# Kernel tuning notes

Hardware: AMD Instinct MI355X
Metric: run time of the kernel (lower is better)

Reference implementation:

```python
import jax, jax.numpy as jnp
import numpy as np

KH, KW = 3, 3
STRIDE = 1
OUT_C = 512


def im2col(x, kh, kw, stride):
    # x: [N, C, H, W] -> col: [C*kh*kw, N*oh*ow]  (row order: C major, then kh, kw)
    N, C, H, W = x.shape
    oh = (H - kh) // stride + 1
    ow = (W - kw) // stride + 1
    rows = jnp.arange(oh)[:, None] * stride + jnp.arange(kh)[None, :]  # [oh, kh]
    cols = jnp.arange(ow)[:, None] * stride + jnp.arange(kw)[None, :]  # [ow, kw]
    # gather windows: result [N, C, oh, kh, ow, kw]
    A = x[:, :, rows[:, :, None, None], cols[None, None, :, :]]
    # permute to (C, kh, kw, N, oh, ow) then flatten, matching torch permute(1,4,5,0,2,3)
    col = jnp.transpose(A, (1, 3, 5, 0, 2, 4)).reshape(C * kh * kw, N * oh * ow)
    return col, oh, ow


def setup_inputs() -> dict:
    key = jax.random.key(0)
    k1, k2, k3 = jax.random.split(key, 3)
    N, C, H, W = 16, 256, 32, 32
    K_sel = (C * KH * KW) // 2  # 1152 rows kept by the binary mask
    x = jax.random.normal(k1, (N, C, H, W), dtype=jnp.float32)
    weight = jax.random.normal(k2, (K_sel, OUT_C), dtype=jnp.float32) * 0.02
    idx = jnp.sort(jax.random.randint(k3, (K_sel,), 0, C * KH * KW, dtype=jnp.int32))
    return {"x": x, "weight": weight, "idx": idx}


def reference(x, weight, idx):
    N = x.shape[0]
    col, oh, ow = im2col(x, KH, KW, STRIDE)          # [C*kh*kw, N*oh*ow]
    x_tile = col[idx, :].T                            # gather masked rows -> [N*oh*ow, K_sel]
    conv_out = x_tile @ weight                        # [N*oh*ow, out_c]
    conv_out = conv_out.reshape(N, oh * ow, OUT_C)
    conv_out = jnp.transpose(conv_out, (0, 2, 1)).reshape(N, OUT_C, oh, ow)
    return conv_out
```

## Files before the change

### kernel.cpp

```cpp
#include <hip/hip_runtime.h>
#include <stdint.h>

#define N_IMG   16
#define C_IN    256
#define H_IN    32
#define W_IN    32
#define OH      30
#define OW      30
#define K_SEL   1152
#define OUTC    512
#define RY_TOT  (N_IMG * OH)
#define M_HAT   (RY_TOT * 32)
#define X_ELEMS (N_IMG * C_IN * H_IN * W_IN)
#define OUT_SP  (OH * OW)
#define CHW     (C_IN * H_IN * W_IN)

#define TO      128
#define TM      64
#define NMT     (M_HAT / TM)
#define NOT     (OUTC / TO)
#define BSTR    40
#define KITER   (K_SEL / 32)

typedef float f32x4  __attribute__((ext_vector_type(4)));
typedef short bf16x8 __attribute__((ext_vector_type(8)));

__device__ __forceinline__ unsigned short f2bf(float f) {
    unsigned int u = __float_as_uint(f);
    u += 0x7FFFu + ((u >> 16) & 1u);
    return (unsigned short)(u >> 16);
}

__device__ __forceinline__ void gl_lds16(const void* g, void* lds) {
    __builtin_amdgcn_global_load_lds(
        (const __attribute__((address_space(1))) unsigned int*)g,
        (__attribute__((address_space(3))) unsigned int*)lds,
        16, 0, 0);
}

__global__ void prep_kernel(const int* __restrict__ idx, const float* __restrict__ w,
                            int* __restrict__ koff, unsigned short* __restrict__ wT) {
    __shared__ float tile[32][33];
    const int bx = blockIdx.x, by = blockIdx.y, t = threadIdx.x;

    if (by == 0) {
        int k = bx * 256 + t;
        if (k < K_SEL) {
            int v = idx[k];
            int c = v / 9, rem = v - c * 9;
            int i = rem / 3, j = rem - i * 3;
            koff[k] = c * (H_IN * W_IN) + i * W_IN + j;
        }
    }
    const int s0 = bx * 32, o0 = by * 32;
    const int oc = t & 31, sg = t >> 5;
#pragma unroll
    for (int i = 0; i < 4; ++i) {
        int sl = sg * 4 + i;
        tile[sl][oc] = w[(s0 + sl) * OUTC + o0 + oc];
    }
    __syncthreads();
    const int ol = t >> 3, sq = t & 7;
    unsigned int u0 = (unsigned int)f2bf(tile[sq * 4 + 0][ol]) |
                      ((unsigned int)f2bf(tile[sq * 4 + 1][ol]) << 16);
    unsigned int u1 = (unsigned int)f2bf(tile[sq * 4 + 2][ol]) |
                      ((unsigned int)f2bf(tile[sq * 4 + 3][ol]) << 16);
    uint2 pk; pk.x = u0; pk.y = u1;
    *reinterpret_cast<uint2*>(&wT[(size_t)(o0 + ol) * K_SEL + s0 + sq * 4]) = pk;
}

__global__ __launch_bounds__(256, 4)
void gemm_kernel(const unsigned short* __restrict__ wT, const float* __restrict__ x,
                 const int* __restrict__ koff, float* __restrict__ out) {
    __shared__ __align__(16) unsigned short As[TO * 32];
    __shared__ __align__(16) unsigned short Bs[TM * BSTR];
    __shared__ int koS[K_SEL];

    const int t    = threadIdx.x;
    const int wave = t >> 6;
    const int lane = t & 63;
    const int quad = lane >> 4;
    const int lo   = lane & 15;

    const int bid = blockIdx.x;
    const int mt  = bid % NMT;
    const int ot  = bid / NMT;
    const int oBase = ot * TO;
    const int mBase = mt * TM;

    for (int i = t; i < K_SEL; i += 256) koS[i] = koff[i];

    int base[2];
#pragma unroll
    for (int ry = 0; ry < 2; ++ry) {
        int ryg = mt * 2 + ry;
        int n = ryg / 30, y = ryg - n * 30;
        base[ry] = n * CHW + y * W_IN;
    }

    const int xw  = t & 31;
    const int kq4 = t >> 5;
    const int ks  = kq4 * 4;

    const int lrow = lane >> 2, lks = (lane & 3) * 8;
    const unsigned short* wrow0 = wT + (size_t)(oBase + wave * 32 + lrow) * K_SEL + lks;
    const unsigned short* wrow1 = wrow0 + (size_t)16 * K_SEL;
    unsigned short* lA0 = &As[(wave * 32) * 32];
    unsigned short* lA1 = lA0 + 16 * 32;

    __syncthreads();

    f32x4 acc[2][4] = {};
    int   kk[2][4];
    float v[2][2][4];

#pragma unroll
    for (int j = 0; j < 4; ++j) kk[0][j] = koS[ks + j];
#pragma unroll
    for (int ry = 0; ry < 2; ++ry)
#pragma unroll
        for (int j = 0; j < 4; ++j) {
            int g = base[ry] + kk[0][j] + xw;
            g = min(g, X_ELEMS - 1);
            v[0][ry][j] = x[g];
        }

#pragma unroll 2
    for (int kt = 0; kt < KITER; ++kt) {
        const int p = kt & 1, q = p ^ 1;
        const int k0 = kt * 32;
        gl_lds16(wrow0 + k0, lA0);
        gl_lds16(wrow1 + k0, lA1);
#pragma unroll
        for (int ry = 0; ry < 2; ++ry) {
            unsigned int u0 = (unsigned int)f2bf(v[p][ry][0]) |
                              ((unsigned int)f2bf(v[p][ry][1]) << 16);
            unsigned int u1 = (unsigned int)f2bf(v[p][ry][2]) |
                              ((unsigned int)f2bf(v[p][ry][3]) << 16);
            uint2 pk; pk.x = u0; pk.y = u1;
            *reinterpret_cast<uint2*>(&Bs[(ry * 32 + xw) * BSTR + ks]) = pk;
        }
        if (kt + 1 < KITER) {
            const int k1 = k0 + 32;
#pragma unroll
            for (int j = 0; j < 4; ++j) kk[q][j] = koS[k1 + ks + j];
#pragma unroll
            for (int ry = 0; ry < 2; ++ry)
#pragma unroll
                for (int j = 0; j < 4; ++j) {
                    int g = base[ry] + kk[q][j] + xw;
                    g = min(g, X_ELEMS - 1);
                    v[q][ry][j] = x[g];
                }
        }
        __syncthreads();

        bf16x8 a[2], b[4];
#pragma unroll
        for (int ms = 0; ms < 2; ++ms)
            a[ms] = *(const bf16x8*)&As[(wave * 32 + ms * 16 + lo) * 32 + quad * 8];
#pragma unroll
        for (int ns = 0; ns < 4; ++ns)
            b[ns] = *(const bf16x8*)&Bs[(ns * 16 + lo) * BSTR + quad * 8];
#pragma unroll
        for (int ms = 0; ms < 2; ++ms)
#pragma unroll
            for (int ns = 0; ns < 4; ++ns)
                acc[ms][ns] = __builtin_amdgcn_mfma_f32_16x16x32_bf16(
                    a[ms], b[ns], acc[ms][ns], 0, 0, 0);
        __syncthreads();
    }

#pragma unroll
    for (int ns = 0; ns < 4; ++ns) {
        const int mh  = mBase + ns * 16 + lo;
        const int xwe = mh & 31;
        const int ryg = mh >> 5;
        const int n = ryg / 30, y = ryg - n * 30;
        if (xwe < OW) {
            const size_t ob = (size_t)n * (OUTC * OUT_SP) + (size_t)y * OW + xwe;
#pragma unroll
            for (int ms = 0; ms < 2; ++ms) {
                const int o0 = oBase + wave * 32 + ms * 16 + quad * 4;
#pragma unroll
                for (int r = 0; r < 4; ++r)
                    out[ob + (size_t)(o0 + r) * OUT_SP] = acc[ms][ns][r];
            }
        }
    }
}

extern "C" void kernel_launch(void* const* d_in, const int* in_sizes, int n_in,
                              void* d_out, int out_size, void* d_ws, size_t ws_size,
                              hipStream_t stream) {
    const float* x   = (const float*)d_in[0];
    const float* w   = (const float*)d_in[1];
    const int*   idx = (const int*)d_in[2];
    float*       out = (float*)d_out;

    char* ws = (char*)d_ws;
    int*            koff = (int*)ws;
    unsigned short* wT   = (unsigned short*)(ws + 4608);

    prep_kernel<<<dim3(K_SEL / 32, OUTC / 32), dim3(256), 0, stream>>>(idx, w, koff, wT);
    gemm_kernel<<<dim3(NMT * NOT), dim3(256), 0, stream>>>(wT, x, koff, out);
}
```

Baseline: 113.5 us.

## Double output-channel tile to 256 and reorder gather prefetch before LDS store

Widens the per-block output-channel tile from 128 to 256, so each wave computes a 64x64 accumulator block and the gathered im2col activations are reused across twice as many output channels. This halves redundant x gathers and bf16 conversions across blocks. It also loads the koff offsets as int4, issues the next-iteration x gather before writing the current B tile, and uses the HIP float2-to-bf16 conversion intrinsic. In exchange, register pressure rises, the occupancy hint drops from 4 to 2, and the grid shrinks to 480 blocks, which may leave some CUs with uneven work.

```diff
diff --git a/kernel.cpp b/kernel.cpp
--- a/kernel.cpp
+++ b/kernel.cpp
@@ -1,4 +1,5 @@
 #include <hip/hip_runtime.h>
+#include <hip/hip_bf16.h>
 #include <stdint.h>
 
 #define N_IMG   16
@@ -15,7 +16,7 @@
 #define OUT_SP  (OH * OW)
 #define CHW     (C_IN * H_IN * W_IN)
 
-#define TO      128
+#define TO      256
 #define TM      64
 #define NMT     (M_HAT / TM)
 #define NOT     (OUTC / TO)
@@ -69,12 +70,12 @@
     *reinterpret_cast<uint2*>(&wT[(size_t)(o0 + ol) * K_SEL + s0 + sq * 4]) = pk;
 }
 
-__global__ __launch_bounds__(256, 4)
+__global__ __launch_bounds__(256, 2)
 void gemm_kernel(const unsigned short* __restrict__ wT, const float* __restrict__ x,
                  const int* __restrict__ koff, float* __restrict__ out) {
     __shared__ __align__(16) unsigned short As[TO * 32];
     __shared__ __align__(16) unsigned short Bs[TM * BSTR];
-    __shared__ int koS[K_SEL];
+    __shared__ __align__(16) int koS[K_SEL];
 
     const int t    = threadIdx.x;
     const int wave = t >> 6;
@@ -90,80 +91,74 @@
 
     for (int i = t; i < K_SEL; i += 256) koS[i] = koff[i];
 
-    int base[2];
+    const int xw  = t & 31;
+    const int ks  = (t >> 5) * 4;
+
+    int bxy[2];
 #pragma unroll
     for (int ry = 0; ry < 2; ++ry) {
         int ryg = mt * 2 + ry;
         int n = ryg / 30, y = ryg - n * 30;
-        base[ry] = n * CHW + y * W_IN;
-    }
-
-    const int xw  = t & 31;
-    const int kq4 = t >> 5;
-    const int ks  = kq4 * 4;
-
-    const int lrow = lane >> 2, lks = (lane & 3) * 8;
-    const unsigned short* wrow0 = wT + (size_t)(oBase + wave * 32 + lrow) * K_SEL + lks;
-    const unsigned short* wrow1 = wrow0 + (size_t)16 * K_SEL;
-    unsigned short* lA0 = &As[(wave * 32) * 32];
-    unsigned short* lA1 = lA0 + 16 * 32;
+        bxy[ry] = n * CHW + y * W_IN + xw;
+    }
+
+    const unsigned short* wrowB = wT + (size_t)(oBase + wave * 16 + (lane >> 2)) * K_SEL
+                                     + (lane & 3) * 8;
+    unsigned short* lA = &As[(wave * 16) * 32];
 
     __syncthreads();
 
-    f32x4 acc[2][4] = {};
-    int   kk[2][4];
+    f32x4 acc[4][4] = {};
+    int4  kk[2];
     float v[2][2][4];
 
-#pragma unroll
-    for (int j = 0; j < 4; ++j) kk[0][j] = koS[ks + j];
-#pragma unroll
-    for (int ry = 0; ry < 2; ++ry)
-#pragma unroll
-        for (int j = 0; j < 4; ++j) {
-            int g = base[ry] + kk[0][j] + xw;
-            g = min(g, X_ELEMS - 1);
-            v[0][ry][j] = x[g];
-        }
-
-#pragma unroll 2
+    kk[0] = *reinterpret_cast<const int4*>(&koS[ks]);
+#pragma unroll
+    for (int ry = 0; ry < 2; ++ry) {
+        v[0][ry][0] = x[min(bxy[ry] + kk[0].x, X_ELEMS - 1)];
+        v[0][ry][1] = x[min(bxy[ry] + kk[0].y, X_ELEMS - 1)];
+        v[0][ry][2] = x[min(bxy[ry] + kk[0].z, X_ELEMS - 1)];
+        v[0][ry][3] = x[min(bxy[ry] + kk[0].w, X_ELEMS - 1)];
+    }
+
     for (int kt = 0; kt < KITER; ++kt) {
         const int p = kt & 1, q = p ^ 1;
         const int k0 = kt * 32;
-        gl_lds16(wrow0 + k0, lA0);
-        gl_lds16(wrow1 + k0, lA1);
+#pragma unroll
+        for (int i = 0; i < 4; ++i)
+            gl_lds16(wrowB + (size_t)i * 64 * K_SEL + k0, lA + i * 64 * 32);
+
+        if (kt + 1 < KITER) {
+            kk[q] = *reinterpret_cast<const int4*>(&koS[k0 + 32 + ks]);
+#pragma unroll
+            for (int ry = 0; ry < 2; ++ry) {
+                v[q][ry][0] = x[min(bxy[ry] + kk[q].x, X_ELEMS - 1)];
+                v[q][ry][1] = x[min(bxy[ry] + kk[q].y, X_ELEMS - 1)];
+                v[q][ry][2] = x[min(bxy[ry] + kk[q].z, X_ELEMS - 1)];
+                v[q][ry][3] = x[min(bxy[ry] + kk[q].w, X_ELEMS - 1)];
+            }
+        }
 #pragma unroll
         for (int ry = 0; ry < 2; ++ry) {
-            unsigned int u0 = (unsigned int)f2bf(v[p][ry][0]) |
-                              ((unsigned int)f2bf(v[p][ry][1]) << 16);
-            unsigned int u1 = (unsigned int)f2bf(v[p][ry][2]) |
-                              ((unsigned int)f2bf(v[p][ry][3]) << 16);
+            __hip_bfloat162 h0 = __float22bfloat162_rn({v[p][ry][0], v[p][ry][1]});
+            __hip_bfloat162 h1 = __float22bfloat162_rn({v[p][ry][2], v[p][ry][3]});
+            unsigned int u0, u1;
+            __builtin_memcpy(&u0, &h0, 4);
+            __builtin_memcpy(&u1, &h1, 4);
             uint2 pk; pk.x = u0; pk.y = u1;
             *reinterpret_cast<uint2*>(&Bs[(ry * 32 + xw) * BSTR + ks]) = pk;
         }
-        if (kt + 1 < KITER) {
-            const int k1 = k0 + 32;
-#pragma unroll
-            for (int j = 0; j < 4; ++j) kk[q][j] = koS[k1 + ks + j];
-#pragma unroll
-            for (int ry = 0; ry < 2; ++ry)
-#pragma unroll
-                for (int j = 0; j < 4; ++j) {
-                    int g = base[ry] + kk[q][j] + xw;
-                    g = min(g, X_ELEMS - 1);
-                    v[q][ry][j] = x[g];
-                }
-        }
         __syncthreads();
 
-        bf16x8 a[2], b[4];
-#pragma unroll
-        for (int ms = 0; ms < 2; ++ms)
-            a[ms] = *(const bf16x8*)&As[(wave * 32 + ms * 16 + lo) * 32 + quad * 8];
+        bf16x8 a[4], b[4];
+#pragma unroll
+        for (int ms = 0; ms < 4; ++ms)
+            a[ms] = *(const bf16x8*)&As[(wave * 64 + ms * 16 + lo) * 32 + quad * 8];
 #pragma unroll
         for (int ns = 0; ns < 4; ++ns)
             b[ns] = *(const bf16x8*)&Bs[(ns * 16 + lo) * BSTR + quad * 8];
 #pragma unroll
-        for (int ms = 0; ms < 2; ++ms)
+        for (int ms = 0; ms < 4; ++ms)
 #pragma unroll
             for (int ns = 0; ns < 4; ++ns)
                 acc[ms][ns] = __builtin_amdgcn_mfma_f32_16x16x32_bf16(
@@ -180,8 +175,8 @@
         if (xwe < OW) {
             const size_t ob = (size_t)n * (OUTC * OUT_SP) + (size_t)y * OW + xwe;
 #pragma unroll
-            for (int ms = 0; ms < 2; ++ms) {
-                const int o0 = oBase + wave * 32 + ms * 16 + quad * 4;
+            for (int ms = 0; ms < 4; ++ms) {
+                const int o0 = oBase + wave * 64 + ms * 16 + quad * 4;
 #pragma unroll
                 for (int r = 0; r < 4; ++r)
                     out[ob + (size_t)(o0 + r) * OUT_SP] = acc[ms][ns][r];
```

Result: slower. 144.3 us (+27.2%).

## Double-buffer LDS tiles and prefetch gathered inputs two stages ahead

Applied to the files above, without the earlier changes.

The single LDS A/B tiles become two ping-pong buffers. Each k-step now stages the next tile (async weight loads plus the bf16-packed gathered inputs) while MFMAs run on the current buffer, and the global gather for the tile after that is issued early. This removes one of the two barriers per iteration and hides more global and LDS latency behind compute. In exchange it doubles the A/B shared memory, which can lower occupancy, and it changes how each wave splits the weight-row loads.

```diff
diff --git a/kernel.cpp b/kernel.cpp
--- a/kernel.cpp
+++ b/kernel.cpp
@@ -1,4 +1,5 @@
 #include <hip/hip_runtime.h>
+#include <hip/hip_bf16.h>
 #include <stdint.h>
 
 #define N_IMG   16
@@ -72,9 +73,9 @@
 __global__ __launch_bounds__(256, 4)
 void gemm_kernel(const unsigned short* __restrict__ wT, const float* __restrict__ x,
                  const int* __restrict__ koff, float* __restrict__ out) {
-    __shared__ __align__(16) unsigned short As[TO * 32];
-    __shared__ __align__(16) unsigned short Bs[TM * BSTR];
-    __shared__ int koS[K_SEL];
+    __shared__ __align__(16) unsigned short As[2][TO * 32];
+    __shared__ __align__(16) unsigned short Bs[2][TM * BSTR];
+    __shared__ __align__(16) int koS[K_SEL];
 
     const int t    = threadIdx.x;
     const int wave = t >> 6;
@@ -90,85 +91,100 @@
 
     for (int i = t; i < K_SEL; i += 256) koS[i] = koff[i];
 
-    int base[2];
+    const int xw = t & 31;
+    const int ks = (t >> 5) * 4;
+
+    int bxy[2];
 #pragma unroll
     for (int ry = 0; ry < 2; ++ry) {
         int ryg = mt * 2 + ry;
         int n = ryg / 30, y = ryg - n * 30;
-        base[ry] = n * CHW + y * W_IN;
-    }
-
-    const int xw  = t & 31;
-    const int kq4 = t >> 5;
-    const int ks  = kq4 * 4;
+        bxy[ry] = n * CHW + y * W_IN + xw;
+    }
 
     const int lrow = lane >> 2, lks = (lane & 3) * 8;
-    const unsigned short* wrow0 = wT + (size_t)(oBase + wave * 32 + lrow) * K_SEL + lks;
-    const unsigned short* wrow1 = wrow0 + (size_t)16 * K_SEL;
-    unsigned short* lA0 = &As[(wave * 32) * 32];
-    unsigned short* lA1 = lA0 + 16 * 32;
+    const unsigned short* wrow0 = wT + (size_t)(oBase + wave * 16 + lrow) * K_SEL + lks;
+    const unsigned short* wrow1 = wrow0 + (size_t)64 * K_SEL;
+    const int lA0 = (wave * 16) * 32;
+    const int lA1 = (64 + wave * 16) * 32;
 
     __syncthreads();
 
     f32x4 acc[2][4] = {};
-    int   kk[2][4];
     float v[2][2][4];
-
-#pragma unroll
-    for (int j = 0; j < 4; ++j) kk[0][j] = koS[ks + j];
-#pragma unroll
-    for (int ry = 0; ry < 2; ++ry)
-#pragma unroll
-        for (int j = 0; j < 4; ++j) {
-            int g = base[ry] + kk[0][j] + xw;
-            g = min(g, X_ELEMS - 1);
-            v[0][ry][j] = x[g];
-        }
-
-#pragma unroll 2
+    int4  kk;
+
+    kk = *reinterpret_cast<const int4*>(&koS[ks]);
+#pragma unroll
+    for (int ry = 0; ry < 2; ++ry) {
+        v[0][ry][0] = x[min(bxy[ry] + kk.x, X_ELEMS - 1)];
+        v[0][ry][1] = x[min(bxy[ry] + kk.y, X_ELEMS - 1)];
+        v[0][ry][2] = x[min(bxy[ry] + kk.z, X_ELEMS - 1)];
+        v[0][ry][3] = x[min(bxy[ry] + kk.w, X_ELEMS - 1)];
+    }
+    gl_lds16(wrow0, &As[0][lA0]);
+    gl_lds16(wrow1, &As[0][lA1]);
+#pragma unroll
+    for (int ry = 0; ry < 2; ++ry) {
+        __hip_bfloat162 h0 = __float22bfloat162_rn({v[0][ry][0], v[0][ry][1]});
+        __hip_bfloat162 h1 = __float22bfloat162_rn({v[0][ry][2], v[0][ry][3]});
+        uint2 pk;
+        __builtin_memcpy(&pk.x, &h0, 4);
+        __builtin_memcpy(&pk.y, &h1, 4);
+        *reinterpret_cast<uint2*>(&Bs[0][(ry * 32 + xw) * BSTR + ks]) = pk;
+    }
+    kk = *reinterpret_cast<const int4*>(&koS[32 + ks]);
+#pragma unroll
+    for (int ry = 0; ry < 2; ++ry) {
+        v[1][ry][0] = x[min(bxy[ry] + kk.x, X_ELEMS - 1)];
+        v[1][ry][1] = x[min(bxy[ry] + kk.y, X_ELEMS - 1)];
+        v[1][ry][2] = x[min(bxy[ry] + kk.z, X_ELEMS - 1)];
+        v[1][ry][3] = x[min(bxy[ry] + kk.w, X_ELEMS - 1)];
+    }
+    __syncthreads();
+
     for (int kt = 0; kt < KITER; ++kt) {
         const int p = kt & 1, q = p ^ 1;
-        const int k0 = kt * 32;
-        gl_lds16(wrow0 + k0, lA0);
-        gl_lds16(wrow1 + k0, lA1);
-#pragma unroll
-        for (int ry = 0; ry < 2; ++ry) {
-            unsigned int u0 = (unsigned int)f2bf(v[p][ry][0]) |
-                              ((unsigned int)f2bf(v[p][ry][1]) << 16);
-            unsigned int u1 = (unsigned int)f2bf(v[p][ry][2]) |
-                              ((unsigned int)f2bf(v[p][ry][3]) << 16);
-            uint2 pk; pk.x = u0; pk.y = u1;
-            *reinterpret_cast<uint2*>(&Bs[(ry * 32 + xw) * BSTR + ks]) = pk;
-        }
         if (kt + 1 < KITER) {
-            const int k1 = k0 + 32;
-#pragma unroll
-            for (int j = 0; j < 4; ++j) kk[q][j] = koS[k1 + ks + j];
-#pragma unroll
-            for (int ry = 0; ry < 2; ++ry)
-#pragma unroll
-                for (int j = 0; j < 4; ++j) {
-                    int g = base[ry] + kk[q][j] + xw;
-                    g = min(g, X_ELEMS - 1);
-                    v[q][ry][j] = x[g];
-                }
-        }
-        __syncthreads();
+            const int k1 = (kt + 1) * 32;
+            gl_lds16(wrow0 + k1, &As[q][lA0]);
+            gl_lds16(wrow1 + k1, &As[q][lA1]);
+#pragma unroll
+            for (int ry = 0; ry < 2; ++ry) {
+                __hip_bfloat162 h0 = __float22bfloat162_rn({v[q][ry][0], v[q][ry][1]});
+                __hip_bfloat162 h1 = __float22bfloat162_rn({v[q][ry][2], v[q][ry][3]});
+                uint2 pk;
+                __builtin_memcpy(&pk.x, &h0, 4);
+                __builtin_memcpy(&pk.y, &h1, 4);
+                *reinterpret_cast<uint2*>(&Bs[q][(ry * 32 + xw) * BSTR + ks]) = pk;
+            }
+        }
+        if (kt + 2 < KITER) {
+            kk = *reinterpret_cast<const int4*>(&koS[(kt + 2) * 32 + ks]);
+#pragma unroll
+            for (int ry = 0; ry < 2; ++ry) {
+                v[p][ry][0] = x[min(bxy[ry] + kk.x, X_ELEMS - 1)];
+                v[p][ry][1] = x[min(bxy[ry] + kk.y, X_ELEMS - 1)];
+                v[p][ry][2] = x[min(bxy[ry] + kk.z, X_ELEMS - 1)];
+                v[p][ry][3] = x[min(bxy[ry] + kk.w, X_ELEMS - 1)];
+            }
+        }
 
         bf16x8 a[2], b[4];
 #pragma unroll
         for (int ms = 0; ms < 2; ++ms)
-            a[ms] = *(const bf16x8*)&As[(wave * 32 + ms * 16 + lo) * 32 + quad * 8];
+            a[ms] = *(const bf16x8*)&As[p][(wave * 32 + ms * 16 + lo) * 32 + quad * 8];
 #pragma unroll
         for (int ns = 0; ns < 4; ++ns)
-            b[ns] = *(const bf16x8*)&Bs[(ns * 16 + lo) * BSTR + quad * 8];
+            b[ns] = *(const bf16x8*)&Bs[p][(ns * 16 + lo) * BSTR + quad * 8];
 #pragma unroll
         for (int ms = 0; ms < 2; ++ms)
 #pragma unroll
             for (int ns = 0; ns < 4; ++ns)
                 acc[ms][ns] = __builtin_amdgcn_mfma_f32_16x16x32_bf16(
                     a[ms], b[ns], acc[ms][ns], 0, 0, 0);
-        __syncthreads();
+
+        if (kt + 1 < KITER) __syncthreads();
     }
 
 #pragma unroll
```

Result: slower. 129.8 us (+14.4%).
